# Performance work log

Hardware: AMD Instinct MI355X
Metric: run time of the kernel (lower is better)

## Reference

```python
import jax, jax.numpy as jnp
import numpy as np

NUM_EDGE_TYPES = 38
DIM = 30
NUM_FEATS = NUM_EDGE_TYPES * DIM  # 1140
N_PAIRS = 50000


def setup_inputs() -> dict:
    key = jax.random.key(0)
    k1, k2, k3 = jax.random.split(key, 3)
    start_emb = jax.random.normal(k1, (N_PAIRS, NUM_FEATS), dtype=jnp.float32)
    end_emb = jax.random.normal(k2, (N_PAIRS, NUM_FEATS), dtype=jnp.float32)
    weights = jax.random.normal(k3, (NUM_EDGE_TYPES, NUM_FEATS, NUM_FEATS), dtype=jnp.float32)
    return {"start_emb": start_emb, "end_emb": end_emb, "weights": weights}


def reference(start_emb, end_emb, weights):
    # Original: for each edge type n, output[n] = diag(start @ W_n @ end.T)
    # i.e. output[n, i] = start[i] . W_n . end[i]. Computed directly per-row
    # (same math, no NxN materialization):
    # [e, n_pairs] <- sum_j (start @ W_e)[i, j] * end[i, j]
    proj = jnp.einsum('ni,eij->enj', start_emb, weights)  # [E, N, F]
    out = jnp.einsum('enj,nj->en', proj, end_emb)          # [E, N]
    return out
```

## Files before the change

### kernel.cpp

```cpp
#include <hip/hip_runtime.h>

#define NUM_E 38
#define FDIM 1140
#define NPAIRS 50000
#define FPAD 1152
#define NPAD 50048
#define BM 128
#define BN 128
#define BJ 32
#define NCHUNK 9
#define NJIT 36
#define NTILES 391

typedef short short8 __attribute__((ext_vector_type(8)));
typedef short short4v __attribute__((ext_vector_type(4)));
typedef float float4v __attribute__((ext_vector_type(4)));

__device__ __forceinline__ short f2bf(float f) {
  union { float f; unsigned u; } v; v.f = f;
  unsigned r = v.u + 0x7FFFu + ((v.u >> 16) & 1u);
  return (short)(r >> 16);
}
__device__ __forceinline__ float bf2f(short s) {
  union { unsigned u; float f; } v; v.u = ((unsigned)(unsigned short)s) << 16;
  return v.f;
}
__device__ __forceinline__ void gl2lds16(const short* g, short* l) {
  __builtin_amdgcn_global_load_lds(
      (const __attribute__((address_space(1))) void*)g,
      (__attribute__((address_space(3))) void*)l, 16, 0, 0);
}

__global__ void __launch_bounds__(256) convpad_kernel(
    const float* __restrict__ src, short* __restrict__ dst,
    int R, int Rpad, int C, int Cpad, int groups)
{
  const int cpc = Cpad >> 3;
  const long total = (long)groups * Rpad * cpc;
  for (long idx = (long)blockIdx.x * blockDim.x + threadIdx.x; idx < total;
       idx += (long)gridDim.x * blockDim.x) {
    const int g   = (int)(idx / ((long)Rpad * cpc));
    const long rem = idx - (long)g * Rpad * cpc;
    const int row = (int)(rem / cpc);
    const int j0  = ((int)(rem - (long)row * cpc)) << 3;
    short8 o = (short8){0,0,0,0,0,0,0,0};
    if (row < R) {
      const float* s = src + ((size_t)g * R + row) * C + j0;
      if (j0 + 8 <= C) {
        float4v v0 = *(const float4v*)s;
        float4v v1 = *(const float4v*)(s + 4);
        o = (short8){f2bf(v0[0]), f2bf(v0[1]), f2bf(v0[2]), f2bf(v0[3]),
                     f2bf(v1[0]), f2bf(v1[1]), f2bf(v1[2]), f2bf(v1[3])};
      } else {
#pragma unroll
        for (int t = 0; t < 8; ++t)
          o[t] = (j0 + t < C) ? f2bf(s[t]) : (short)0;
      }
    }
    *(short8*)(dst + ((size_t)g * Rpad + row) * Cpad + j0) = o;
  }
}

template <int PP>
__device__ __forceinline__ void nc_group(
    const short* __restrict__ Abase,
    const short* __restrict__ Bbase,
    const short* __restrict__ Sbase,
    float (&out_acc)[16],
    short* lds_a, short* lds_b, float* lds_red,
    int k0, int wave, int lane)
{
  const int l15  = lane & 15;
  const int quad = lane >> 4;
  const int wr   = wave >> 1;
  const int wc   = wave & 1;
  const int sr   = lane >> 2;
  const int scz  = ((lane & 3) ^ ((lane >> 3) & 3)) << 3;
  const int rc   = (quad ^ ((l15 >> 1) & 3)) << 3;
  const int a_off = (((wr << 6) + l15) << 5) + rc;
  const int b_off = (((wc << 6) + l15) << 5) + rc;

  float4v acc[PP][4][4];
#pragma unroll
  for (int p = 0; p < PP; ++p)
#pragma unroll
    for (int mi = 0; mi < 4; ++mi)
#pragma unroll
      for (int ni = 0; ni < 4; ++ni)
        acc[p][mi][ni] = (float4v){0.f, 0.f, 0.f, 0.f};

  for (int jt = 0; jt < NJIT; ++jt) {
    const int j0 = jt << 5;
#pragma unroll
    for (int rd = 0; rd < 2; ++rd) {
      const int slab = (wave << 1) + rd;
      gl2lds16(Abase + (size_t)((slab << 4) + sr) * FPAD + j0 + scz,
               lds_a + (slab << 9));
    }
#pragma unroll
    for (int rd = 0; rd < 2 * PP; ++rd) {
      const int bslab = wave * (2 * PP) + rd;
      gl2lds16(Bbase + (size_t)(k0 + (bslab << 4) + sr) * FPAD + j0 + scz,
               lds_b + (bslab << 9));
    }
    __syncthreads();

    short8 af[4], bfr[PP][4];
#pragma unroll
    for (int mi = 0; mi < 4; ++mi)
      af[mi] = *(const short8*)(lds_a + a_off + (mi << 9));
#pragma unroll
    for (int p = 0; p < PP; ++p)
#pragma unroll
      for (int ni = 0; ni < 4; ++ni)
        bfr[p][ni] = *(const short8*)(lds_b + (p << 12) + b_off + (ni << 9));

#pragma unroll
    for (int p = 0; p < PP; ++p)
#pragma unroll
      for (int mi = 0; mi < 4; ++mi)
#pragma unroll
        for (int ni = 0; ni < 4; ++ni)
          acc[p][mi][ni] = __builtin_amdgcn_mfma_f32_16x16x32_bf16(
              af[mi], bfr[p][ni], acc[p][mi][ni], 0, 0, 0);
    __syncthreads();
  }

#pragma unroll
  for (int p = 0; p < PP; ++p) {
#pragma unroll
    for (int mi = 0; mi < 4; ++mi) {
#pragma unroll
      for (int r = 0; r < 4; ++r) {
        const int il = (wr << 6) + (mi << 4) + (quad << 2) + r;
        const short* srow = Sbase + (size_t)il * FPAD + k0 + (p << 7) + (wc << 6);
        float s = 0.f;
#pragma unroll
        for (int ni = 0; ni < 4; ++ni)
          s += acc[p][mi][ni][r] * bf2f(srow[(ni << 4) + l15]);
        s += __shfl_xor(s, 1);
        s += __shfl_xor(s, 2);
        s += __shfl_xor(s, 4);
        s += __shfl_xor(s, 8);
        if (wc == 0) {
          out_acc[(mi << 2) + r] += s;
        } else if (l15 == 0) {
          lds_red[il] = s;
        }
      }
    }
    __syncthreads();
    if (wc == 0) {
#pragma unroll
      for (int mi = 0; mi < 4; ++mi)
#pragma unroll
        for (int r = 0; r < 4; ++r)
          out_acc[(mi << 2) + r] +=
              lds_red[(wr << 6) + (mi << 4) + (quad << 2) + r];
    }
    __syncthreads();
  }
}

__global__ void __launch_bounds__(256, 2) kway_bf16_kernel(
    const short* __restrict__ Wbf,
    const short* __restrict__ Sbf,
    const short* __restrict__ Ebf,
    float* __restrict__ out)
{
  __shared__ short lds_a[BM * BJ];
  __shared__ short lds_b[2 * BM * BJ];
  __shared__ float lds_red[BM];

  const int e  = blockIdx.x / NTILES;
  const int it = blockIdx.x % NTILES;
  const int i0 = it * BM;

  const int tid  = threadIdx.x;
  const int wave = tid >> 6;
  const int lane = tid & 63;

  const short* Abase = Ebf + (size_t)i0 * FPAD;
  const short* Bbase = Wbf + (size_t)e * FPAD * FPAD;
  const short* Sbase = Sbf + (size_t)i0 * FPAD;

  float out_acc[16];
#pragma unroll
  for (int x = 0; x < 16; ++x) out_acc[x] = 0.f;

  for (int g = 0; g < 4; ++g)
    nc_group<2>(Abase, Bbase, Sbase, out_acc, lds_a, lds_b, lds_red,
                g << 8, wave, lane);
  nc_group<1>(Abase, Bbase, Sbase, out_acc, lds_a, lds_b, lds_red,
              1024, wave, lane);

  if ((wave & 1) == 0 && (lane & 15) == 0) {
    const int wr = wave >> 1;
    const int quad = lane >> 4;
#pragma unroll
    for (int mi = 0; mi < 4; ++mi)
#pragma unroll
      for (int r = 0; r < 4; ++r) {
        const int gi = i0 + (wr << 6) + (mi << 4) + (quad << 2) + r;
        if (gi < NPAIRS) out[(size_t)e * NPAIRS + gi] = out_acc[(mi << 2) + r];
      }
  }
}

#define LSTRIDE 40
__global__ void __launch_bounds__(256) kway_fp32_kernel(
    const float* __restrict__ start_emb,
    const float* __restrict__ end_emb,
    const float* __restrict__ weights,
    float* __restrict__ out)
{
  __shared__ short lds_a[BM * LSTRIDE];
  __shared__ short lds_b[BN * LSTRIDE];

  const int e  = blockIdx.x % NUM_E;
  const int it = blockIdx.x / NUM_E;
  const int i0 = it * BM;

  const int tid  = threadIdx.x;
  const int wave = tid >> 6;
  const int lane = tid & 63;
  const int l15  = lane & 15;
  const int quad = lane >> 4;

  const float* We = weights + (size_t)e * FDIM * FDIM;
  const int srow = tid >> 3;
  const int scol = (tid & 7) << 2;

  float out_acc[8];
#pragma unroll
  for (int x = 0; x < 8; ++x) out_acc[x] = 0.f;

  for (int nc = 0; nc < NCHUNK; ++nc) {
    const int k0 = nc * BN;
    float4v acc[2][8];
#pragma unroll
    for (int mi = 0; mi < 2; ++mi)
#pragma unroll
      for (int ni = 0; ni < 8; ++ni)
        acc[mi][ni] = (float4v){0.f, 0.f, 0.f, 0.f};

    for (int jt = 0; jt < NJIT; ++jt) {
      const int gj = jt * BJ + scol;
      const bool jok = gj < FDIM;
      float4v av[4], bv[4];
#pragma unroll
      for (int rr = 0; rr < 4; ++rr) {
        const int row = (rr << 5) + srow;
        const int gi = i0 + row;
        av[rr] = (float4v){0.f, 0.f, 0.f, 0.f};
        if (jok && gi < NPAIRS)
          av[rr] = *(const float4v*)(end_emb + (size_t)gi * FDIM + gj);
        const int gk = k0 + row;
        bv[rr] = (float4v){0.f, 0.f, 0.f, 0.f};
        if (jok && gk < FDIM)
          bv[rr] = *(const float4v*)(We + (size_t)gk * FDIM + gj);
      }
#pragma unroll
      for (int rr = 0; rr < 4; ++rr) {
        const int row = (rr << 5) + srow;
        short4v a4 = { f2bf(av[rr][0]), f2bf(av[rr][1]), f2bf(av[rr][2]), f2bf(av[rr][3]) };
        *(short4v*)(&lds_a[row * LSTRIDE + scol]) = a4;
        short4v b4 = { f2bf(bv[rr][0]), f2bf(bv[rr][1]), f2bf(bv[rr][2]), f2bf(bv[rr][3]) };
        *(short4v*)(&lds_b[row * LSTRIDE + scol]) = b4;
      }
      __syncthreads();

      short8 afrag[2], bfrag[8];
#pragma unroll
      for (int mi = 0; mi < 2; ++mi)
        afrag[mi] = *(short8*)(&lds_a[((wave << 5) + (mi << 4) + l15) * LSTRIDE + (quad << 3)]);
#pragma unroll
      for (int ni = 0; ni < 8; ++ni)
        bfrag[ni] = *(short8*)(&lds_b[((ni << 4) + l15) * LSTRIDE + (quad << 3)]);
#pragma unroll
      for (int mi = 0; mi < 2; ++mi)
#pragma unroll
        for (int ni = 0; ni < 8; ++ni)
          acc[mi][ni] = __builtin_amdgcn_mfma_f32_16x16x32_bf16(
              afrag[mi], bfrag[ni], acc[mi][ni], 0, 0, 0);
      __syncthreads();
    }

#pragma unroll
    for (int mi = 0; mi < 2; ++mi) {
#pragma unroll
      for (int r = 0; r < 4; ++r) {
        const int gi = i0 + (wave << 5) + (mi << 4) + (quad << 2) + r;
        const bool iok = gi < NPAIRS;
        float s = 0.f;
#pragma unroll
        for (int ni = 0; ni < 8; ++ni) {
          const int k = k0 + (ni << 4) + l15;
          const float sv = (iok && k < FDIM) ? start_emb[(size_t)gi * FDIM + k] : 0.f;
          s += acc[mi][ni][r] * sv;
        }
        out_acc[(mi << 2) + r] += s;
      }
    }
  }

#pragma unroll
  for (int x = 0; x < 8; ++x) {
    float v = out_acc[x];
    v += __shfl_xor(v, 1);
    v += __shfl_xor(v, 2);
    v += __shfl_xor(v, 4);
    v += __shfl_xor(v, 8);
    out_acc[x] = v;
  }
  if (l15 == 0) {
#pragma unroll
    for (int mi = 0; mi < 2; ++mi)
#pragma unroll
      for (int r = 0; r < 4; ++r) {
        const int gi = i0 + (wave << 5) + (mi << 4) + (quad << 2) + r;
        if (gi < NPAIRS) out[(size_t)e * NPAIRS + gi] = out_acc[(mi << 2) + r];
      }
  }
}

extern "C" void kernel_launch(void* const* d_in, const int* in_sizes, int n_in,
                              void* d_out, int out_size, void* d_ws, size_t ws_size,
                              hipStream_t stream) {
  const float* start_emb = (const float*)d_in[0];
  const float* end_emb   = (const float*)d_in[1];
  const float* weights   = (const float*)d_in[2];
  float* out = (float*)d_out;

  const size_t W_ELEMS = (size_t)NUM_E * FPAD * FPAD;
  const size_t EMB_ELEMS = (size_t)NPAD * FPAD;
  const size_t need = (W_ELEMS + 2 * EMB_ELEMS) * sizeof(short);

  if (ws_size >= need) {
    short* Wbf = (short*)d_ws;
    short* Sbf = Wbf + W_ELEMS;
    short* Ebf = Sbf + EMB_ELEMS;

    {
      const long wt = (long)NUM_E * FPAD * (FPAD >> 3);
      convpad_kernel<<<(int)((wt + 255) / 256), 256, 0, stream>>>(
          weights, Wbf, FDIM, FPAD, FDIM, FPAD, NUM_E);
      const long et = (long)NPAD * (FPAD >> 3);
      convpad_kernel<<<(int)((et + 255) / 256), 256, 0, stream>>>(
          start_emb, Sbf, NPAIRS, NPAD, FDIM, FPAD, 1);
      convpad_kernel<<<(int)((et + 255) / 256), 256, 0, stream>>>(
          end_emb, Ebf, NPAIRS, NPAD, FDIM, FPAD, 1);
    }
    kway_bf16_kernel<<<NUM_E * NTILES, 256, 0, stream>>>(Wbf, Sbf, Ebf, out);
  } else {
    kway_fp32_kernel<<<NUM_E * NTILES, 256, 0, stream>>>(
        start_emb, end_emb, weights, out);
  }
}
```

Before: 7.527 ms.

## Double-buffer LDS tiles to overlap global-to-LDS loads with MFMA compute

Doubles the LDS buffers for the A and B tiles and prefetches the next j-tile into the alternate buffer while the current one feeds the MFMAs. Partial vmcnt waits replace the full syncthreads drain, so global load latency can hide behind compute. Global row pointers are also hoisted out of the j loop. The cost is twice the LDS per block, which may limit occupancy (launch bounds target 2 blocks per CU), and the hand-written waitcnt count must match the number of loads issued per stage.

```diff
diff --git a/kernel.cpp b/kernel.cpp
--- a/kernel.cpp
+++ b/kernel.cpp
@@ -80,6 +80,15 @@
   const int a_off = (((wr << 6) + l15) << 5) + rc;
   const int b_off = (((wc << 6) + l15) << 5) + rc;
 
+  const short* ga[2];
+  const short* gb[2 * PP];
+#pragma unroll
+  for (int rd = 0; rd < 2; ++rd)
+    ga[rd] = Abase + (size_t)((((wave << 1) + rd) << 4) + sr) * FPAD + scz;
+#pragma unroll
+  for (int rd = 0; rd < 2 * PP; ++rd)
+    gb[rd] = Bbase + (size_t)(k0 + ((wave * 2 * PP + rd) << 4) + sr) * FPAD + scz;
+
   float4v acc[PP][4][4];
 #pragma unroll
   for (int p = 0; p < PP; ++p)
@@ -89,32 +98,30 @@
       for (int ni = 0; ni < 4; ++ni)
         acc[p][mi][ni] = (float4v){0.f, 0.f, 0.f, 0.f};
 
-  for (int jt = 0; jt < NJIT; ++jt) {
-    const int j0 = jt << 5;
-#pragma unroll
-    for (int rd = 0; rd < 2; ++rd) {
-      const int slab = (wave << 1) + rd;
-      gl2lds16(Abase + (size_t)((slab << 4) + sr) * FPAD + j0 + scz,
-               lds_a + (slab << 9));
-    }
-#pragma unroll
-    for (int rd = 0; rd < 2 * PP; ++rd) {
-      const int bslab = wave * (2 * PP) + rd;
-      gl2lds16(Bbase + (size_t)(k0 + (bslab << 4) + sr) * FPAD + j0 + scz,
-               lds_b + (bslab << 9));
-    }
-    __syncthreads();
-
+  auto stage = [&](int jtn, int buf) {
+    const int j0 = jtn << 5;
+    short* la = lds_a + (buf << 12);
+    short* lb = lds_b + buf * (PP << 12);
+#pragma unroll
+    for (int rd = 0; rd < 2; ++rd)
+      gl2lds16(ga[rd] + j0, la + (((wave << 1) + rd) << 9));
+#pragma unroll
+    for (int rd = 0; rd < 2 * PP; ++rd)
+      gl2lds16(gb[rd] + j0, lb + ((wave * 2 * PP + rd) << 9));
+  };
+
+  auto compute = [&](int buf) {
+    const short* la = lds_a + (buf << 12);
+    const short* lb = lds_b + buf * (PP << 12);
     short8 af[4], bfr[PP][4];
 #pragma unroll
     for (int mi = 0; mi < 4; ++mi)
-      af[mi] = *(const short8*)(lds_a + a_off + (mi << 9));
+      af[mi] = *(const short8*)(la + a_off + (mi << 9));
 #pragma unroll
     for (int p = 0; p < PP; ++p)
 #pragma unroll
       for (int ni = 0; ni < 4; ++ni)
-        bfr[p][ni] = *(const short8*)(lds_b + (p << 12) + b_off + (ni << 9));
-
+        bfr[p][ni] = *(const short8*)(lb + (p << 12) + b_off + (ni << 9));
 #pragma unroll
     for (int p = 0; p < PP; ++p)
 #pragma unroll
@@ -123,8 +130,22 @@
         for (int ni = 0; ni < 4; ++ni)
           acc[p][mi][ni] = __builtin_amdgcn_mfma_f32_16x16x32_bf16(
               af[mi], bfr[p][ni], acc[p][mi][ni], 0, 0, 0);
-    __syncthreads();
-  }
+  };
+
+  stage(0, 0);
+  int cur = 0;
+  for (int jt = 0; jt < NJIT - 1; ++jt) {
+    stage(jt + 1, cur ^ 1);
+    asm volatile("s_waitcnt vmcnt(%0)" :: "i"(2 + 2 * PP) : "memory");
+    __builtin_amdgcn_s_barrier();
+    compute(cur);
+    __builtin_amdgcn_s_barrier();
+    cur ^= 1;
+  }
+  asm volatile("s_waitcnt vmcnt(0)" ::: "memory");
+  __builtin_amdgcn_s_barrier();
+  compute(cur);
+  __builtin_amdgcn_s_barrier();
 
 #pragma unroll
   for (int p = 0; p < PP; ++p) {
@@ -168,8 +189,8 @@
     const short* __restrict__ Ebf,
     float* __restrict__ out)
 {
-  __shared__ short lds_a[BM * BJ];
-  __shared__ short lds_b[2 * BM * BJ];
+  __shared__ short lds_a[2 * BM * BJ];
+  __shared__ short lds_b[2 * 2 * BM * BJ];
   __shared__ float lds_red[BM];
 
   const int e  = blockIdx.x / NTILES;
```

Measured after the change: 7.513 ms. Within noise of the previous version (-0.2%).
